# Performance work log

Measured on AMD Instinct MI355X. Metric: run time of the kernel, lower is better.

The kernel has to match this reference:

```python
import jax, jax.numpy as jnp
import numpy as np

B, S, D = 4, 2048, 2048
E = 8            # num_experts
TOP_K = 2
H = 1408         # intermediate_size per expert
SH = 2 * H       # shared expert intermediate (shared_experts=2)


def setup_inputs() -> dict:
    key = jax.random.key(0)
    ks = jax.random.split(key, 8)
    sc = 0.02
    return {
        "hidden_states": jax.random.normal(ks[0], (B, S, D), jnp.float32),
        "gate_w": jax.random.normal(ks[1], (E, D), jnp.float32) * sc,   # torch Linear weight [out,in]
        "w1": jax.random.normal(ks[2], (E, H, D), jnp.float32) * sc,    # gate_proj per expert
        "w3": jax.random.normal(ks[3], (E, H, D), jnp.float32) * sc,    # up_proj per expert
        "w2": jax.random.normal(ks[4], (E, D, H), jnp.float32) * sc,    # down_proj per expert
        "sw1": jax.random.normal(ks[5], (SH, D), jnp.float32) * sc,
        "sw3": jax.random.normal(ks[6], (SH, D), jnp.float32) * sc,
        "sw2": jax.random.normal(ks[7], (D, SH), jnp.float32) * sc,
    }


def reference(hidden_states, gate_w, w1, w3, w2, sw1, sw3, sw2):
    b, s, d = hidden_states.shape
    x = hidden_states.reshape(-1, d)                      # [T, D]
    logits = x @ gate_w.T                                 # [T, E]
    rw, sel = jax.lax.top_k(logits, TOP_K)                # [T, K]
    rw = jax.nn.softmax(rw, axis=-1)                      # norm_topk_prob=True
    onehot = jax.nn.one_hot(sel, E, dtype=x.dtype)        # [T, K, E]
    token_mask = onehot.sum(axis=1)                       # [T, E] in {0,1}
    # NOTE: faithful to the source quirk: expert_weights.sum(dim=-1) on a flat
    # masked gather sums routing weights over ALL tokens selecting the expert,
    # producing one scalar per expert.
    s_e = (rw[..., None] * onehot).sum(axis=(0, 1))       # [E]
    combine = token_mask * s_e                            # [T, E]
    # per-expert SwiGLU MLP on all tokens (dense combine form of gather/scatter)
    g = jnp.einsum('td,ehd->eth', x, w1)                  # [E, T, H]
    u = jnp.einsum('td,ehd->eth', x, w3)
    a = jax.nn.silu(g) * u
    y = jnp.einsum('eth,edh->etd', a, w2)                 # [E, T, D]
    out = jnp.einsum('te,etd->td', combine, y)            # [T, D]
    shared = (jax.nn.silu(x @ sw1.T) * (x @ sw3.T)) @ sw2.T
    out = out + shared
    return out.reshape(b, s, d)
```

## Files before the change

kernel.cpp:

```cpp
#include <hip/hip_runtime.h>
#include <hip/hip_bf16.h>
#include <stdint.h>

#define T_TOK 8192
#define DIM   2048
#define NEXP  8
#define HDIM  1408
#define SHDIM 2816

typedef __attribute__((ext_vector_type(8))) short bfrag;
typedef __attribute__((ext_vector_type(4))) float f32x4;
typedef __attribute__((ext_vector_type(4))) short s16x4;

__device__ __forceinline__ short f2bf(float f) {
    union { float f; uint32_t u; } v; v.f = f;
    return (short)((v.u + 0x8000u) >> 16);
}
__device__ __forceinline__ float bf2f(short s) {
    union { uint32_t u; float f; } v; v.u = ((uint32_t)(uint16_t)s) << 16;
    return v.f;
}

__device__ __forceinline__ bfrag cvt8(float4 a, float4 b) {
    bfrag r;
    r[0] = f2bf(a.x); r[1] = f2bf(a.y); r[2] = f2bf(a.z); r[3] = f2bf(a.w);
    r[4] = f2bf(b.x); r[5] = f2bf(b.y); r[6] = f2bf(b.z); r[7] = f2bf(b.w);
    return r;
}

__device__ __forceinline__ void gload16(const void* g, void* l) {
    __builtin_amdgcn_global_load_lds(
        (__attribute__((address_space(1))) void*)(g),
        (__attribute__((address_space(3))) void*)(l), 16, 0, 0);
}

#define MFMA16(a, b, c) __builtin_amdgcn_mfma_f32_16x16x32_bf16((a), (b), (c), 0, 0, 0)


__global__ __launch_bounds__(256) void gate_kernel(
    const float* __restrict__ x, const float* __restrict__ gw,
    __hip_bfloat16* __restrict__ xbf,
    int* __restrict__ sel, int* __restrict__ meta, float* __restrict__ s_e)
{
    __shared__ float g[NEXP * DIM];
    for (int i = threadIdx.x; i < NEXP * DIM; i += 256) g[i] = gw[i];
    __syncthreads();
    const int wid = threadIdx.x >> 6, lane = threadIdx.x & 63;
    for (int it = 0; it < 8; ++it) {
        const int t = blockIdx.x * 32 + wid * 8 + it;
        float acc[NEXP];
#pragma unroll
        for (int e = 0; e < NEXP; ++e) acc[e] = 0.f;
        const float4* xr = (const float4*)(x + (size_t)t * DIM);
        for (int j = 0; j < DIM / 4; j += 64) {
            float4 xv = xr[j + lane];
            s16x4 xv16 = { f2bf(xv.x), f2bf(xv.y), f2bf(xv.z), f2bf(xv.w) };
            *(s16x4*)&xbf[(size_t)t * DIM + (j + lane) * 4] = xv16;
#pragma unroll
            for (int e = 0; e < NEXP; ++e) {
                float4 gv = *(const float4*)&g[e * DIM + (j + lane) * 4];
                acc[e] += xv.x * gv.x + xv.y * gv.y + xv.z * gv.z + xv.w * gv.w;
            }
        }
#pragma unroll
        for (int e = 0; e < NEXP; ++e)
            for (int o = 32; o; o >>= 1) acc[e] += __shfl_xor(acc[e], o);
        if (lane == 0) {
            int e0 = 0; float v0 = acc[0];
#pragma unroll
            for (int e = 1; e < NEXP; ++e) if (acc[e] > v0) { v0 = acc[e]; e0 = e; }
            int e1 = -1; float v1 = -3.4e38f;
#pragma unroll
            for (int e = 0; e < NEXP; ++e) if (e != e0 && acc[e] > v1) { v1 = acc[e]; e1 = e; }
            float p0 = 1.f / (1.f + __expf(v1 - v0));
            float p1 = 1.f - p0;
            sel[2 * t] = e0; sel[2 * t + 1] = e1;
            atomicAdd(&s_e[e0], p0); atomicAdd(&s_e[e1], p1);
            atomicAdd(&meta[e0], 1); atomicAdd(&meta[e1], 1);
        }
    }
}

__global__ void scan_kernel(int* meta) {
    if (threadIdx.x == 0) {
        int acc = 0;
        for (int e = 0; e < NEXP; ++e) {
            meta[16 + e] = acc;
            meta[8 + e]  = acc;
            acc += meta[e];
        }
        meta[24] = acc;
    }
}

__global__ __launch_bounds__(256) void fill_kernel(
    const int* __restrict__ sel, int* __restrict__ meta,
    int* __restrict__ list, int2* __restrict__ slots)
{
    const int t = blockIdx.x * 256 + threadIdx.x;
    int e0 = sel[2 * t], e1 = sel[2 * t + 1];
    int p0 = atomicAdd(&meta[8 + e0], 1); list[p0] = t;
    int p1 = atomicAdd(&meta[8 + e1], 1); list[p1] = t;
    slots[t] = make_int2(p0, p1);
}

#define C1 2883584
#define C2 5767168
#define C3 8650752
#define C4 9371648
#define C5 10092544
#define C6 10813440
__global__ __launch_bounds__(256) void cvt6_kernel(
    const float* __restrict__ s0, const float* __restrict__ s1, const float* __restrict__ s2,
    const float* __restrict__ s3, const float* __restrict__ s4, const float* __restrict__ s5,
    __hip_bfloat16* __restrict__ d0, __hip_bfloat16* __restrict__ d1, __hip_bfloat16* __restrict__ d2,
    __hip_bfloat16* __restrict__ d3, __hip_bfloat16* __restrict__ d4, __hip_bfloat16* __restrict__ d5)
{
    const int stride = gridDim.x * 256;
    for (int i = blockIdx.x * 256 + threadIdx.x; i < C6; i += stride) {
        const float* s; __hip_bfloat16* d; int off;
        if      (i < C1) { s = s0; d = d0; off = i; }
        else if (i < C2) { s = s1; d = d1; off = i - C1; }
        else if (i < C3) { s = s2; d = d2; off = i - C2; }
        else if (i < C4) { s = s3; d = d3; off = i - C3; }
        else if (i < C5) { s = s4; d = d4; off = i - C4; }
        else             { s = s5; d = d5; off = i - C5; }
        const float4* p = (const float4*)(s + (size_t)off * 8);
        float4 a = p[0], b = p[1];
        *(bfrag*)(d + (size_t)off * 8) = cvt8(a, b);
    }
}


template<int N, bool GATHER>
__device__ __forceinline__ void up_core(
    const __hip_bfloat16* __restrict__ X,
    const __hip_bfloat16* __restrict__ B1p,
    const __hip_bfloat16* __restrict__ B3p,
    __hip_bfloat16* __restrict__ actp,
    const int* __restrict__ list,
    int base, int count, int m0, int n0, short* lds)
{
    constexpr int K = DIM;
    constexpr int NT = K / 64;
    short (*As)[256 * 64]  = (short (*)[256 * 64])lds;
    short (*B1s)[128 * 64] = (short (*)[128 * 64])(lds + 32768);
    short (*B3s)[128 * 64] = (short (*)[128 * 64])(lds + 49152);

    const int tid = threadIdx.x, wid = tid >> 6, lane = tid & 63;
    const int rlo = lane >> 3;
    const int swslot = (lane & 7) ^ rlo;

    const __hip_bfloat16* pA[4];
#pragma unroll
    for (int q = 0; q < 4; ++q) {
        int row = (q * 8 + wid) * 8 + rlo;
        int r = m0 + row; if (r > count - 1) r = count - 1;
        int ga = GATHER ? list[base + r] : r;
        pA[q] = X + (size_t)ga * K + swslot * 8;
    }
    const __hip_bfloat16* pB1[2];
    const __hip_bfloat16* pB3[2];
#pragma unroll
    for (int q = 0; q < 2; ++q) {
        int row = (q * 8 + wid) * 8 + rlo;
        pB1[q] = B1p + (size_t)(n0 + row) * K + swslot * 8;
        pB3[q] = B3p + (size_t)(n0 + row) * K + swslot * 8;
    }

#define STAGE_UP(T, BUF) do { const int k0_ = (T) * 64;                         \
    _Pragma("unroll") for (int q = 0; q < 4; ++q)                               \
        gload16(pA[q] + k0_, &As[BUF][(q * 8 + wid) * 512]);                    \
    _Pragma("unroll") for (int q = 0; q < 2; ++q) {                             \
        gload16(pB1[q] + k0_, &B1s[BUF][(q * 8 + wid) * 512]);                  \
        gload16(pB3[q] + k0_, &B3s[BUF][(q * 8 + wid) * 512]); } } while (0)

    const int wm = wid >> 2, wn = wid & 3;
    const int l15 = lane & 15, lhi = lane >> 4;

    f32x4 accg[8][2], accu[8][2];
#pragma unroll
    for (int i = 0; i < 8; ++i)
#pragma unroll
        for (int j = 0; j < 2; ++j) { accg[i][j] = 0.f; accu[i][j] = 0.f; }

    STAGE_UP(0, 0);
    __syncthreads();
    int cur = 0;
#pragma unroll 1
    for (int t = 0; t < NT; ++t) {
        if (t + 1 < NT) STAGE_UP(t + 1, cur ^ 1);
        __builtin_amdgcn_sched_barrier(0);
        bfrag b1f[2][2], b3f[2][2];
#pragma unroll
        for (int j = 0; j < 2; ++j)
#pragma unroll
            for (int kk = 0; kk < 2; ++kk) {
                int rb = wn * 32 + j * 16 + l15;
                int c = kk * 4 + lhi;
                int off = rb * 128 + ((c ^ (rb & 7)) << 4);
                b1f[j][kk] = *(const bfrag*)((const char*)B1s[cur] + off);
                b3f[j][kk] = *(const bfrag*)((const char*)B3s[cur] + off);
            }
        __builtin_amdgcn_s_setprio(1);
#pragma unroll
        for (int i = 0; i < 8; ++i) {
            int ra = wm * 128 + i * 16 + l15;
            const char* abase = (const char*)As[cur] + ra * 128;
            bfrag a0 = *(const bfrag*)(abase + ((lhi       ^ (ra & 7)) << 4));
            bfrag a1 = *(const bfrag*)(abase + (((4 + lhi) ^ (ra & 7)) << 4));
#pragma unroll
            for (int j = 0; j < 2; ++j) {
                accg[i][j] = MFMA16(a0, b1f[j][0], accg[i][j]);
                accu[i][j] = MFMA16(a0, b3f[j][0], accu[i][j]);
                accg[i][j] = MFMA16(a1, b1f[j][1], accg[i][j]);
                accu[i][j] = MFMA16(a1, b3f[j][1], accu[i][j]);
            }
        }
        __builtin_amdgcn_s_setprio(0);
        __syncthreads();
        cur ^= 1;
    }
#undef STAGE_UP

#pragma unroll
    for (int i = 0; i < 8; ++i)
#pragma unroll
        for (int r = 0; r < 4; ++r) {
            int m = wm * 128 + i * 16 + lhi * 4 + r;
            if (m0 + m < count) {
#pragma unroll
                for (int j = 0; j < 2; ++j) {
                    float gg = accg[i][j][r];
                    float uu = accu[i][j][r];
                    float a = gg / (1.f + __expf(-gg)) * uu;
                    int n = n0 + wn * 32 + j * 16 + l15;
                    actp[(size_t)(base + m0 + m) * N + n] = __float2bfloat16(a);
                }
            }
        }
}

template<int KD, bool TO_BF16>
__device__ __forceinline__ void down_core(
    const __hip_bfloat16* __restrict__ Ap,
    const __hip_bfloat16* __restrict__ Bp,
    float* __restrict__ out, __hip_bfloat16* __restrict__ yscr,
    int base, int count, int m0, int n0, short* lds)
{
    constexpr int NT = KD / 64;
    short (*As)[256 * 64] = (short (*)[256 * 64])lds;
    short (*Bs)[256 * 64] = (short (*)[256 * 64])(lds + 32768);

    const int tid = threadIdx.x, wid = tid >> 6, lane = tid & 63;
    const int rlo = lane >> 3;
    const int swslot = (lane & 7) ^ rlo;

    const __hip_bfloat16* pA[4];
    const __hip_bfloat16* pB[4];
#pragma unroll
    for (int q = 0; q < 4; ++q) {
        int row = (q * 8 + wid) * 8 + rlo;
        int r = m0 + row; if (r > count - 1) r = count - 1;
        pA[q] = Ap + (size_t)(base + r) * KD + swslot * 8;
        pB[q] = Bp + (size_t)(n0 + row) * KD + swslot * 8;
    }

#define STAGE_DN(T, BUF) do { const int k0_ = (T) * 64;                         \
    _Pragma("unroll") for (int q = 0; q < 4; ++q) {                             \
        gload16(pA[q] + k0_, &As[BUF][(q * 8 + wid) * 512]);                    \
        gload16(pB[q] + k0_, &Bs[BUF][(q * 8 + wid) * 512]); } } while (0)

    const int wm = wid >> 2, wn = wid & 3;
    const int l15 = lane & 15, lhi = lane >> 4;

    f32x4 acc[8][4];
#pragma unroll
    for (int i = 0; i < 8; ++i)
#pragma unroll
        for (int j = 0; j < 4; ++j) acc[i][j] = 0.f;

    STAGE_DN(0, 0);
    __syncthreads();
    int cur = 0;
#pragma unroll 1
    for (int t = 0; t < NT; ++t) {
        if (t + 1 < NT) STAGE_DN(t + 1, cur ^ 1);
        __builtin_amdgcn_sched_barrier(0);
        bfrag bf[4][2];
#pragma unroll
        for (int j = 0; j < 4; ++j)
#pragma unroll
            for (int kk = 0; kk < 2; ++kk) {
                int rb = wn * 64 + j * 16 + l15;
                int c = kk * 4 + lhi;
                bf[j][kk] = *(const bfrag*)((const char*)Bs[cur] + rb * 128 + ((c ^ (rb & 7)) << 4));
            }
        __builtin_amdgcn_s_setprio(1);
#pragma unroll
        for (int i = 0; i < 8; ++i) {
            int ra = wm * 128 + i * 16 + l15;
            const char* abase = (const char*)As[cur] + ra * 128;
            bfrag a0 = *(const bfrag*)(abase + ((lhi       ^ (ra & 7)) << 4));
            bfrag a1 = *(const bfrag*)(abase + (((4 + lhi) ^ (ra & 7)) << 4));
#pragma unroll
            for (int j = 0; j < 4; ++j) {
                acc[i][j] = MFMA16(a0, bf[j][0], acc[i][j]);
                acc[i][j] = MFMA16(a1, bf[j][1], acc[i][j]);
            }
        }
        __builtin_amdgcn_s_setprio(0);
        __syncthreads();
        cur ^= 1;
    }
#undef STAGE_DN

#pragma unroll
    for (int i = 0; i < 8; ++i)
#pragma unroll
        for (int r = 0; r < 4; ++r) {
            int m = wm * 128 + i * 16 + lhi * 4 + r;
            if (m0 + m < count) {
#pragma unroll
                for (int j = 0; j < 4; ++j) {
                    int n = n0 + wn * 64 + j * 16 + l15;
                    if (TO_BF16)
                        yscr[(size_t)(base + m0 + m) * DIM + n] = __float2bfloat16(acc[i][j][r]);
                    else
                        out[(size_t)(m0 + m) * DIM + n] = acc[i][j][r];
                }
            }
        }
}

template<int N, bool GATHER>
__global__ __launch_bounds__(512, 2) void up_k(
    const __hip_bfloat16* __restrict__ X,
    const __hip_bfloat16* __restrict__ W1, const __hip_bfloat16* __restrict__ W3,
    __hip_bfloat16* __restrict__ act,
    const int* __restrict__ list, const int* __restrict__ meta)
{
    constexpr int nx = N / 128, ny = T_TOK / 256, nz = GATHER ? NEXP : 1;
    constexpr int nwg = nx * ny * nz, cpx = nwg / 8;
    const int bid = (int)blockIdx.x + nx * ((int)blockIdx.y + ny * (int)blockIdx.z);
    const int virt = (bid & 7) * cpx + (bid >> 3);
    const int xi = virt % nx, rest = virt / nx, yi = rest % ny, e = rest / ny;
    int count, base;
    if (GATHER) { count = meta[e]; base = meta[16 + e]; if (yi * 256 >= count) return; }
    else { count = T_TOK; base = 0; }
    __shared__ alignas(16) short lds[65536];
    up_core<N, GATHER>(X, W1 + (size_t)e * N * DIM, W3 + (size_t)e * N * DIM,
                       act, list, base, count, yi * 256, xi * 128, lds);
}

template<int KD, bool TO_BF16>
__global__ __launch_bounds__(512, 2) void down_k(
    const __hip_bfloat16* __restrict__ A, const __hip_bfloat16* __restrict__ W2,
    float* __restrict__ out, __hip_bfloat16* __restrict__ yscr,
    const int* __restrict__ meta)
{
    constexpr int nx = DIM / 256, ny = T_TOK / 256, nz = TO_BF16 ? NEXP : 1;
    constexpr int nwg = nx * ny * nz, cpx = nwg / 8;
    const int bid = (int)blockIdx.x + nx * ((int)blockIdx.y + ny * (int)blockIdx.z);
    const int virt = (bid & 7) * cpx + (bid >> 3);
    const int xi = virt % nx, rest = virt / nx, yi = rest % ny, e = rest / ny;
    int count, base;
    if (TO_BF16) { count = meta[e]; base = meta[16 + e]; if (yi * 256 >= count) return; }
    else { count = T_TOK; base = 0; }
    __shared__ alignas(16) short lds[65536];
    down_core<KD, TO_BF16>(A, W2 + (size_t)e * DIM * KD, out, yscr,
                           base, count, yi * 256, xi * 256, lds);
}

__global__ __launch_bounds__(512, 2) void mid_merged(
    const __hip_bfloat16* __restrict__ act_sh, const __hip_bfloat16* __restrict__ sw2bf,
    float* __restrict__ out,
    const __hip_bfloat16* __restrict__ xbf,
    const __hip_bfloat16* __restrict__ w1bf, const __hip_bfloat16* __restrict__ w3bf,
    __hip_bfloat16* __restrict__ act_ex,
    const int* __restrict__ list, const int* __restrict__ meta)
{
    __shared__ alignas(16) short lds[65536];
    const int bid = (int)blockIdx.x;
    if (bid < 256) {
        constexpr int cpx = 256 / 8;
        const int virt = (bid & 7) * cpx + (bid >> 3);
        const int n0 = (virt & 7) * 256, m0 = (virt >> 3) * 256;
        down_core<SHDIM, false>(act_sh, sw2bf, out, nullptr, 0, T_TOK, m0, n0, lds);
    } else {
        const int b = bid - 256;
        constexpr int cpx = 2816 / 8;
        const int virt = (b & 7) * cpx + (b >> 3);
        const int e = virt / 352, r = virt % 352;
        const int n0 = (r % 11) * 128, m0 = (r / 11) * 256;
        const int count = meta[e], base = meta[16 + e];
        if (m0 >= count) return;
        up_core<HDIM, true>(xbf, w1bf + (size_t)e * HDIM * DIM, w3bf + (size_t)e * HDIM * DIM,
                            act_ex, list, base, count, m0, n0, lds);
    }
}

__global__ __launch_bounds__(256) void combine_kernel(
    float* __restrict__ out, const __hip_bfloat16* __restrict__ yscr,
    const int* __restrict__ sel, const int2* __restrict__ slots,
    const float* __restrict__ s_e)
{
    const int t = blockIdx.x;
    const int d = threadIdx.x * 8;
    const int2 sl = slots[t];
    const float se0 = s_e[sel[2 * t]];
    const float se1 = s_e[sel[2 * t + 1]];
    bfrag y0 = *(const bfrag*)&yscr[(size_t)sl.x * DIM + d];
    bfrag y1 = *(const bfrag*)&yscr[(size_t)sl.y * DIM + d];
    float4* o = (float4*)(out + (size_t)t * DIM + d);
    float4 o0 = o[0], o1 = o[1];
    o0.x += se0 * bf2f(y0[0]) + se1 * bf2f(y1[0]);
    o0.y += se0 * bf2f(y0[1]) + se1 * bf2f(y1[1]);
    o0.z += se0 * bf2f(y0[2]) + se1 * bf2f(y1[2]);
    o0.w += se0 * bf2f(y0[3]) + se1 * bf2f(y1[3]);
    o1.x += se0 * bf2f(y0[4]) + se1 * bf2f(y1[4]);
    o1.y += se0 * bf2f(y0[5]) + se1 * bf2f(y1[5]);
    o1.z += se0 * bf2f(y0[6]) + se1 * bf2f(y1[6]);
    o1.w += se0 * bf2f(y0[7]) + se1 * bf2f(y1[7]);
    o[0] = o0; o[1] = o1;
}

extern "C" void kernel_launch(void* const* d_in, const int* in_sizes, int n_in,
                              void* d_out, int out_size, void* d_ws, size_t ws_size,
                              hipStream_t stream) {
    const float* x   = (const float*)d_in[0];
    const float* gw  = (const float*)d_in[1];
    const float* w1  = (const float*)d_in[2];
    const float* w3  = (const float*)d_in[3];
    const float* w2  = (const float*)d_in[4];
    const float* sw1 = (const float*)d_in[5];
    const float* sw3 = (const float*)d_in[6];
    const float* sw2 = (const float*)d_in[7];
    float* out = (float*)d_out;

    const size_t SZ_X    = (size_t)T_TOK * DIM * 2;
    const size_t SZ_W    = (size_t)NEXP * HDIM * DIM * 2;
    const size_t SZ_SW   = (size_t)SHDIM * DIM * 2;
    const size_t SZ_ACTS = (size_t)T_TOK * SHDIM * 2;
    const size_t SZ_ACTE = (size_t)2 * T_TOK * HDIM * 2;
    const size_t SZ_INTS = (size_t)6 * T_TOK * sizeof(int) + 512;
    const size_t need_base   = SZ_X + 3 * SZ_W + 3 * SZ_SW + SZ_ACTS + SZ_INTS;
    const size_t need_merged = need_base + SZ_ACTE;

    char* p = (char*)d_ws;
    __hip_bfloat16* xbf   = (__hip_bfloat16*)p; p += SZ_X;
    __hip_bfloat16* w1bf  = (__hip_bfloat16*)p; p += SZ_W;
    __hip_bfloat16* w3bf  = (__hip_bfloat16*)p; p += SZ_W;
    __hip_bfloat16* w2bf  = (__hip_bfloat16*)p; p += SZ_W;
    __hip_bfloat16* sw1bf = (__hip_bfloat16*)p; p += SZ_SW;
    __hip_bfloat16* sw3bf = (__hip_bfloat16*)p; p += SZ_SW;
    __hip_bfloat16* sw2bf = (__hip_bfloat16*)p; p += SZ_SW;
    __hip_bfloat16* act_sh = (__hip_bfloat16*)p; p += SZ_ACTS;
    const bool merged = (need_merged <= ws_size);
    __hip_bfloat16* act_ex = merged ? (__hip_bfloat16*)p : act_sh;
    if (merged) p += SZ_ACTE;
    int*  list  = (int*)p;  p += (size_t)2 * T_TOK * sizeof(int);
    int*  sel   = (int*)p;  p += (size_t)2 * T_TOK * sizeof(int);
    int2* slots = (int2*)p; p += (size_t)2 * T_TOK * sizeof(int);
    int*  meta  = (int*)p;
    float* s_e  = (float*)(meta + 32);
    __hip_bfloat16* yscr = (__hip_bfloat16*)d_ws;
    if (need_base > ws_size) return;

    hipMemsetAsync(meta, 0, 256, stream);
    gate_kernel<<<T_TOK / 32, 256, 0, stream>>>(x, gw, xbf, sel, meta, s_e);
    scan_kernel<<<1, 64, 0, stream>>>(meta);
    fill_kernel<<<T_TOK / 256, 256, 0, stream>>>(sel, meta, list, slots);
    cvt6_kernel<<<2048, 256, 0, stream>>>(w1, w3, w2, sw1, sw3, sw2,
                                          w1bf, w3bf, w2bf, sw1bf, sw3bf, sw2bf);

    if (merged) {
        up_k<SHDIM, false><<<dim3(SHDIM / 128, T_TOK / 256, 1), 512, 0, stream>>>(
            xbf, sw1bf, sw3bf, act_sh, nullptr, meta);
        mid_merged<<<256 + 2816, 512, 0, stream>>>(
            act_sh, sw2bf, out, xbf, w1bf, w3bf, act_ex, list, meta);
        down_k<HDIM, true><<<dim3(DIM / 256, T_TOK / 256, NEXP), 512, 0, stream>>>(
            act_ex, w2bf, out, yscr, meta);
    } else {
        up_k<SHDIM, false><<<dim3(SHDIM / 128, T_TOK / 256, 1), 512, 0, stream>>>(
            xbf, sw1bf, sw3bf, act_sh, nullptr, meta);
        down_k<SHDIM, false><<<dim3(DIM / 256, T_TOK / 256, 1), 512, 0, stream>>>(
            act_sh, sw2bf, out, nullptr, meta);
        up_k<HDIM, true><<<dim3(HDIM / 128, T_TOK / 256, NEXP), 512, 0, stream>>>(
            xbf, w1bf, w3bf, act_ex, list, meta);
        down_k<HDIM, true><<<dim3(DIM / 256, T_TOK / 256, NEXP), 512, 0, stream>>>(
            act_ex, w2bf, out, yscr, meta);
    }
    combine_kernel<<<T_TOK, 256, 0, stream>>>(out, yscr, sel, slots, s_e);
}
```

Baseline: 1.000 ms.

## Overlap weight conversion with gate and shared-expert up-projection kernels

The standalone fp32-to-bf16 weight conversion kernel is removed. Shared-expert sw1/sw3 conversion moves into extra blocks of the gate kernel, and the remaining weights (w1, w3, w2, sw2) are converted by extra blocks appended to the shared-expert up-projection GEMM launch. The aim is to hide the bandwidth-bound conversion behind compute work and save launches. The risk is that the converter blocks compete with the GEMM for CUs and memory bandwidth, and that the GEMM blocks must be scheduled before the converters so they are not delayed.

```diff
diff --git a/kernel.cpp b/kernel.cpp
--- a/kernel.cpp
+++ b/kernel.cpp
@@ -37,17 +37,34 @@
 #define MFMA16(a, b, c) __builtin_amdgcn_mfma_f32_16x16x32_bf16((a), (b), (c), 0, 0, 0)
 
 
-__global__ __launch_bounds__(256) void gate_kernel(
+__global__ __launch_bounds__(256) void gate_cvt_kernel(
     const float* __restrict__ x, const float* __restrict__ gw,
     __hip_bfloat16* __restrict__ xbf,
-    int* __restrict__ sel, int* __restrict__ meta, float* __restrict__ s_e)
-{
+    int* __restrict__ sel, int* __restrict__ meta, float* __restrict__ s_e,
+    const float* __restrict__ sw1f, const float* __restrict__ sw3f,
+    __hip_bfloat16* __restrict__ sw1bf, __hip_bfloat16* __restrict__ sw3bf)
+{
+    const int bid = blockIdx.x;
+    if (bid >= T_TOK / 32) {
+        constexpr size_t E_SW = (size_t)SHDIM * DIM;
+        constexpr int NCH = (int)(2 * E_SW / 2048);
+        const int w = bid - T_TOK / 32;
+        for (int c = w; c < NCH; c += 256) {
+            size_t elem = (size_t)c * 2048 + threadIdx.x * 8;
+            const float* s; __hip_bfloat16* d;
+            if (elem < E_SW) { s = sw1f + elem; d = sw1bf + elem; }
+            else             { s = sw3f + (elem - E_SW); d = sw3bf + (elem - E_SW); }
+            float4 a = ((const float4*)s)[0], b = ((const float4*)s)[1];
+            *(bfrag*)d = cvt8(a, b);
+        }
+        return;
+    }
     __shared__ float g[NEXP * DIM];
     for (int i = threadIdx.x; i < NEXP * DIM; i += 256) g[i] = gw[i];
     __syncthreads();
     const int wid = threadIdx.x >> 6, lane = threadIdx.x & 63;
     for (int it = 0; it < 8; ++it) {
-        const int t = blockIdx.x * 32 + wid * 8 + it;
+        const int t = bid * 32 + wid * 8 + it;
         float acc[NEXP];
 #pragma unroll
         for (int e = 0; e < NEXP; ++e) acc[e] = 0.f;
@@ -102,33 +119,6 @@
     int p0 = atomicAdd(&meta[8 + e0], 1); list[p0] = t;
     int p1 = atomicAdd(&meta[8 + e1], 1); list[p1] = t;
     slots[t] = make_int2(p0, p1);
-}
-
-#define C1 2883584
-#define C2 5767168
-#define C3 8650752
-#define C4 9371648
-#define C5 10092544
-#define C6 10813440
-__global__ __launch_bounds__(256) void cvt6_kernel(
-    const float* __restrict__ s0, const float* __restrict__ s1, const float* __restrict__ s2,
-    const float* __restrict__ s3, const float* __restrict__ s4, const float* __restrict__ s5,
-    __hip_bfloat16* __restrict__ d0, __hip_bfloat16* __restrict__ d1, __hip_bfloat16* __restrict__ d2,
-    __hip_bfloat16* __restrict__ d3, __hip_bfloat16* __restrict__ d4, __hip_bfloat16* __restrict__ d5)
-{
-    const int stride = gridDim.x * 256;
-    for (int i = blockIdx.x * 256 + threadIdx.x; i < C6; i += stride) {
-        const float* s; __hip_bfloat16* d; int off;
-        if      (i < C1) { s = s0; d = d0; off = i; }
-        else if (i < C2) { s = s1; d = d1; off = i - C1; }
-        else if (i < C3) { s = s2; d = d2; off = i - C2; }
-        else if (i < C4) { s = s3; d = d3; off = i - C3; }
-        else if (i < C5) { s = s4; d = d4; off = i - C4; }
-        else             { s = s5; d = d5; off = i - C5; }
-        const float4* p = (const float4*)(s + (size_t)off * 8);
-        float4 a = p[0], b = p[1];
-        *(bfrag*)(d + (size_t)off * 8) = cvt8(a, b);
-    }
 }
 
 
@@ -331,6 +321,61 @@
                 }
             }
         }
+}
+
+#define UPSH_NG 704
+#define UPSH_NCVT 512
+__global__ __launch_bounds__(512, 2) void upsh_cvt_k(
+    const __hip_bfloat16* __restrict__ X,
+    const __hip_bfloat16* __restrict__ SW1, const __hip_bfloat16* __restrict__ SW3,
+    __hip_bfloat16* __restrict__ act_sh,
+    const float* __restrict__ w1f, const float* __restrict__ w3f,
+    const float* __restrict__ w2f, const float* __restrict__ sw2f,
+    __hip_bfloat16* __restrict__ w1bf, __hip_bfloat16* __restrict__ w3bf,
+    __hip_bfloat16* __restrict__ w2bf, __hip_bfloat16* __restrict__ sw2bf)
+{
+    const int bid = blockIdx.x;
+    if (bid >= UPSH_NG) {
+        constexpr size_t E_W  = (size_t)NEXP * HDIM * DIM;
+        constexpr size_t E_SW = (size_t)SHDIM * DIM;
+        constexpr int NCH = (int)((3 * E_W + E_SW) / 4096);
+        const int w = bid - UPSH_NG;
+        for (int c = w; c < NCH; c += UPSH_NCVT) {
+            size_t elem = (size_t)c * 4096 + threadIdx.x * 8;
+            const float* s; __hip_bfloat16* d;
+            if      (elem < E_W)          { s = w1f + elem;               d = w1bf + elem; }
+            else if (elem < 2 * E_W)      { s = w3f + (elem - E_W);       d = w3bf + (elem - E_W); }
+            else if (elem < 3 * E_W)      { s = w2f + (elem - 2 * E_W);   d = w2bf + (elem - 2 * E_W); }
+            else                          { s = sw2f + (elem - 3 * E_W);  d = sw2bf + (elem - 3 * E_W); }
+            float4 a = ((const float4*)s)[0], b = ((const float4*)s)[1];
+            *(bfrag*)d = cvt8(a, b);
+        }
+        return;
+    }
+    constexpr int nx = SHDIM / 128, cpx = UPSH_NG / 8;
+    const int virt = (bid & 7) * cpx + (bid >> 3);
+    const int xi = virt % nx, yi = virt / nx;
+    __shared__ alignas(16) short lds[65536];
+    up_core<SHDIM, false>(X, SW1, SW3, act_sh, nullptr, 0, T_TOK, yi * 256, xi * 128, lds);
+}
+
+template<int KD, bool TO_BF16>
+__global__ __launch_bounds__(512, 2) void down_k(
+    const __hip_bfloat16* __restrict__ A, const __hip_bfloat16* __restrict__ W2,
+    float* __restrict__ out, __hip_bfloat16* __restrict__ yscr,
+    const int* __restrict__ meta)
+{
+    constexpr int nx = DIM / 256, ny = T_TOK / 256, nz = TO_BF16 ? NEXP : 1;
+    constexpr int nwg = nx * ny * nz, cpx = nwg / 8;
+    const int bid = (int)blockIdx.x + nx * ((int)blockIdx.y + ny * (int)blockIdx.z);
+    const int virt = (bid & 7) * cpx + (bid >> 3);
+    const int xi = virt % nx, rest = virt / nx, yi = rest % ny, e = rest / ny;
+    int count, base;
+    if (TO_BF16) { count = meta[e]; base = meta[16 + e]; if (yi * 256 >= count) return; }
+    else { count = T_TOK; base = 0; }
+    __shared__ alignas(16) short lds[65536];
+    down_core<KD, TO_BF16>(A, W2 + (size_t)e * DIM * KD, out, yscr,
+                           base, count, yi * 256, xi * 256, lds);
 }
 
 template<int N, bool GATHER>
@@ -351,25 +396,6 @@
     __shared__ alignas(16) short lds[65536];
     up_core<N, GATHER>(X, W1 + (size_t)e * N * DIM, W3 + (size_t)e * N * DIM,
                        act, list, base, count, yi * 256, xi * 128, lds);
-}
-
-template<int KD, bool TO_BF16>
-__global__ __launch_bounds__(512, 2) void down_k(
-    const __hip_bfloat16* __restrict__ A, const __hip_bfloat16* __restrict__ W2,
-    float* __restrict__ out, __hip_bfloat16* __restrict__ yscr,
-    const int* __restrict__ meta)
-{
-    constexpr int nx = DIM / 256, ny = T_TOK / 256, nz = TO_BF16 ? NEXP : 1;
-    constexpr int nwg = nx * ny * nz, cpx = nwg / 8;
-    const int bid = (int)blockIdx.x + nx * ((int)blockIdx.y + ny * (int)blockIdx.z);
-    const int virt = (bid & 7) * cpx + (bid >> 3);
-    const int xi = virt % nx, rest = virt / nx, yi = rest % ny, e = rest / ny;
-    int count, base;
-    if (TO_BF16) { count = meta[e]; base = meta[16 + e]; if (yi * 256 >= count) return; }
-    else { count = T_TOK; base = 0; }
-    __shared__ alignas(16) short lds[65536];
-    down_core<KD, TO_BF16>(A, W2 + (size_t)e * DIM * KD, out, yscr,
-                           base, count, yi * 256, xi * 256, lds);
 }
 
 __global__ __launch_bounds__(512, 2) void mid_merged(
@@ -468,22 +494,20 @@
     if (need_base > ws_size) return;
 
     hipMemsetAsync(meta, 0, 256, stream);
-    gate_kernel<<<T_TOK / 32, 256, 0, stream>>>(x, gw, xbf, sel, meta, s_e);
+    gate_cvt_kernel<<<T_TOK / 32 + 256, 256, 0, stream>>>(
+        x, gw, xbf, sel, meta, s_e, sw1, sw3, sw1bf, sw3bf);
     scan_kernel<<<1, 64, 0, stream>>>(meta);
     fill_kernel<<<T_TOK / 256, 256, 0, stream>>>(sel, meta, list, slots);
-    cvt6_kernel<<<2048, 256, 0, stream>>>(w1, w3, w2, sw1, sw3, sw2,
-                                          w1bf, w3bf, w2bf, sw1bf, sw3bf, sw2bf);
+
+    upsh_cvt_k<<<UPSH_NG + UPSH_NCVT, 512, 0, stream>>>(
+        xbf, sw1bf, sw3bf, act_sh, w1, w3, w2, sw2, w1bf, w3bf, w2bf, sw2bf);
 
     if (merged) {
-        up_k<SHDIM, false><<<dim3(SHDIM / 128, T_TOK / 256, 1), 512, 0, stream>>>(
-            xbf, sw1bf, sw3bf, act_sh, nullptr, meta);
         mid_merged<<<256 + 2816, 512, 0, stream>>>(
             act_sh, sw2bf, out, xbf, w1bf, w3bf, act_ex, list, meta);
         down_k<HDIM, true><<<dim3(DIM / 256, T_TOK / 256, NEXP), 512, 0, stream>>>(
             act_ex, w2bf, out, yscr, meta);
     } else {
-        up_k<SHDIM, false><<<dim3(SHDIM / 128, T_TOK / 256, 1), 512, 0, stream>>>(
-            xbf, sw1bf, sw3bf, act_sh, nullptr, meta);
         down_k<SHDIM, false><<<dim3(DIM / 256, T_TOK / 256, 1), 512, 0, stream>>>(
             act_sh, sw2bf, out, nullptr, meta);
         up_k<HDIM, true><<<dim3(HDIM / 128, T_TOK / 256, NEXP), 512, 0, stream>>>(
```

Measured after the change: 987.8 us. No clear change (-1.3%).
